# Optimization experiments

Measured on AMD Instinct MI355X. Metric: run time of the kernel, lower is better.

The kernel has to match this reference:

```python
import jax, jax.numpy as jnp
import numpy as np

GN_EPS = 1e-5
LN_EPS = 1e-5
M_HEADS, N_LEVELS, N_POINTS, D_MODEL = 8, 3, 4, 256
HEAD_DIM = D_MODEL // M_HEADS


def conv1x1(x, w, b):
    return jnp.einsum('nchw,oc->nohw', x, w[:, :, 0, 0]) + b[None, :, None, None]


def conv3x3(x, w, b):
    y = jax.lax.conv_general_dilated(x, w, (1, 1), ((1, 1), (1, 1)),
                                     dimension_numbers=('NCHW', 'OIHW', 'NCHW'))
    return y + b[None, :, None, None]


def group_norm(x, w, b, groups=32):
    N, C, H, W = x.shape
    xg = x.reshape(N, groups, C // groups, H, W)
    mu = xg.mean((2, 3, 4), keepdims=True)
    var = xg.var((2, 3, 4), keepdims=True)
    xg = (xg - mu) / jnp.sqrt(var + GN_EPS)
    return xg.reshape(N, C, H, W) * w[None, :, None, None] + b[None, :, None, None]


def layer_norm(x, w, b):
    mu = x.mean(-1, keepdims=True)
    var = x.var(-1, keepdims=True)
    return (x - mu) / jnp.sqrt(var + LN_EPS) * w + b


def prelu(x, a):
    return jnp.where(x >= 0, x, a[0] * x)


def pos_sine(mask):
    # DETR PositionEmbeddingSine, num_pos_feats=128, normalize=True
    nm = (~mask).astype(jnp.float32)
    y_embed = jnp.cumsum(nm, 1)
    x_embed = jnp.cumsum(nm, 2)
    eps, scale = 1e-6, 2.0 * np.pi
    y_embed = y_embed / (y_embed[:, -1:, :] + eps) * scale
    x_embed = x_embed / (x_embed[:, :, -1:] + eps) * scale
    npf = D_MODEL // 2
    dim_t = 10000.0 ** (2.0 * (jnp.arange(npf) // 2).astype(jnp.float32) / npf)
    px = x_embed[..., None] / dim_t
    py = y_embed[..., None] / dim_t

    def il(p):
        return jnp.stack([jnp.sin(p[..., 0::2]), jnp.cos(p[..., 1::2])], -1).reshape(p.shape[0], p.shape[1], p.shape[2], -1)

    return jnp.transpose(jnp.concatenate([il(py), il(px)], -1), (0, 3, 1, 2))


def resize_mask_nearest(mask, h, w):
    H, W = mask.shape[1], mask.shape[2]
    iy = jnp.floor(jnp.arange(h) * (H / h)).astype(jnp.int32)
    ix = jnp.floor(jnp.arange(w) * (W / w)).astype(jnp.int32)
    return mask[:, iy][:, :, ix]


def bilinear_gather(v, x, y):
    # v: (N,M,D,H,W); x,y: (N,Lq,M,P) pixel coords; zero padding, align_corners=False
    N, M, D, H, W = v.shape
    Lq, P = x.shape[1], x.shape[3]
    x0f = jnp.floor(x)
    y0f = jnp.floor(y)
    wx = (x - x0f)[..., None]
    wy = (y - y0f)[..., None]
    x0i = x0f.astype(jnp.int32)
    y0i = y0f.astype(jnp.int32)
    flat = jnp.transpose(v, (0, 1, 3, 4, 2)).reshape(N, M, H * W, D)

    def gather(xi, yi):
        valid = (xi >= 0) & (xi < W) & (yi >= 0) & (yi < H)
        idx = jnp.clip(yi, 0, H - 1) * W + jnp.clip(xi, 0, W - 1)
        idx2 = jnp.transpose(idx, (0, 2, 1, 3)).reshape(N, M, Lq * P)
        g = jnp.take_along_axis(flat, idx2[..., None], axis=2)
        g = jnp.transpose(g.reshape(N, M, Lq, P, D), (0, 2, 1, 3, 4))
        return g * valid[..., None]

    g00 = gather(x0i, y0i)
    g01 = gather(x0i + 1, y0i)
    g10 = gather(x0i, y0i + 1)
    g11 = gather(x0i + 1, y0i + 1)
    return g00 * (1 - wx) * (1 - wy) + g01 * wx * (1 - wy) + g10 * (1 - wx) * wy + g11 * wx * wy


def _forward(x0, x1, x2, p3_w, p3_b, p4_w, p4_b, p5_w, p5_b,
             gn3_w, gn3_b, gn4_w, gn4_b, gn5_w, gn5_b, level_embed,
             so_w, so_b, aw_w, aw_b, vp_w, vp_b, op_w, op_b,
             ln1_w, ln1_b, ffn1_w, ffn1_b, ffn2_w, ffn2_b, ln2_w, ln2_b,
             d3_w, d3_b, d3_a, d4_w, d4_b, d4_a, d5_w, d5_b, d5_a,
             padding_masks):
    N = x0.shape[0]
    shapes = [(x0.shape[2], x0.shape[3]), (x1.shape[2], x1.shape[3]), (x2.shape[2], x2.shape[3])]
    p3 = group_norm(conv1x1(x0, p3_w, p3_b), gn3_w, gn3_b)
    p4 = group_norm(conv1x1(x1, p4_w, p4_b), gn4_w, gn4_b)
    p5 = group_norm(conv1x1(x2, p5_w, p5_b), gn5_w, gn5_b)
    srcs = [p3, p4, p5]
    masks = [resize_mask_nearest(padding_masks, H, W) for (H, W) in shapes]
    src_flat = jnp.concatenate([s.reshape(N, D_MODEL, -1).transpose(0, 2, 1) for s in srcs], 1)
    mask_flat = jnp.concatenate([m.reshape(N, -1) for m in masks], 1)
    pos_flat = jnp.concatenate(
        [pos_sine(m).reshape(N, D_MODEL, -1).transpose(0, 2, 1) + level_embed[l][None, None]
         for l, m in enumerate(masks)], 1)
    # valid ratios (N, 3, 2) as (w, h)
    vrs = []
    for (H, W), m in zip(shapes, masks):
        vh = jnp.sum((~m[:, :, 0]).astype(jnp.float32), 1) / H
        vw = jnp.sum((~m[:, 0, :]).astype(jnp.float32), 1) / W
        vrs.append(jnp.stack([vw, vh], -1))
    vr = jnp.stack(vrs, 1)
    # reference points (N, Lq, 3, 2)
    refs = []
    for lvl, (H, W) in enumerate(shapes):
        ry, rx = jnp.meshgrid(jnp.linspace(0.5, H - 0.5, H), jnp.linspace(0.5, W - 0.5, W), indexing='ij')
        ry = ry.reshape(-1)[None] / (vr[:, None, lvl, 1] * H)
        rx = rx.reshape(-1)[None] / (vr[:, None, lvl, 0] * W)
        refs.append(jnp.stack([rx, ry], -1))
    ref = jnp.concatenate(refs, 1)[:, :, None] * vr[:, None]

    # --- MSDeformAttn ---
    q = src_flat + pos_flat
    Lq = q.shape[1]
    value = src_flat @ vp_w.T + vp_b
    value = jnp.where(mask_flat[..., None], 0.0, value).reshape(N, Lq, M_HEADS, HEAD_DIM)
    off = (q @ so_w.T + so_b).reshape(N, Lq, M_HEADS, N_LEVELS, N_POINTS, 2)
    aw = jax.nn.softmax((q @ aw_w.T + aw_b).reshape(N, Lq, M_HEADS, N_LEVELS * N_POINTS), -1)
    aw = aw.reshape(N, Lq, M_HEADS, N_LEVELS, N_POINTS)
    norm = jnp.array([[W, H] for (H, W) in shapes], jnp.float32)
    loc = ref[:, :, None, :, None, :] + off / norm[None, None, None, :, None, :]
    out = jnp.zeros((N, Lq, M_HEADS, HEAD_DIM), value.dtype)
    start = 0
    for l, (H, W) in enumerate(shapes):
        vl = value[:, start:start + H * W].reshape(N, H, W, M_HEADS, HEAD_DIM)
        vl = jnp.transpose(vl, (0, 3, 4, 1, 2))  # (N, M, D, H, W)
        sx = loc[:, :, :, l, :, 0] * W - 0.5
        sy = loc[:, :, :, l, :, 1] * H - 0.5
        samp = bilinear_gather(vl, sx, sy)  # (N, Lq, M, P, D)
        out = out + jnp.einsum('nqmpd,nqmp->nqmd', samp, aw[:, :, :, l])
        start += H * W
    attn = out.reshape(N, Lq, D_MODEL) @ op_w.T + op_b

    src = layer_norm(src_flat + attn, ln1_w, ln1_b)
    ffn = jax.nn.relu(src @ ffn1_w.T + ffn1_b) @ ffn2_w.T + ffn2_b
    src = layer_norm(src + ffn, ln2_w, ln2_b)

    # take level-2 tokens back to spatial
    H2, W2 = shapes[2]
    start2 = shapes[0][0] * shapes[0][1] + shapes[1][0] * shapes[1][1]
    o = src[:, start2:start2 + H2 * W2].reshape(N, H2, W2, D_MODEL).transpose(0, 3, 1, 2)

    o = jax.image.resize(o, (N, D_MODEL) + shapes[0], 'bilinear', antialias=False) + prelu(conv3x3(x0, d3_w, d3_b), d3_a)
    o = jax.image.resize(o, (N, D_MODEL) + shapes[1], 'bilinear', antialias=False) + prelu(conv3x3(x1, d4_w, d4_b), d4_a)
    o = jax.image.resize(o, (N, D_MODEL) + shapes[2], 'bilinear', antialias=False) + prelu(conv3x3(x2, d5_w, d5_b), d5_a)
    return o


def setup_inputs():
    key = jax.random.key(0)
    ks = jax.random.split(key, 24)
    B, C = 2, 256

    def w(k, shape, sc=0.02):
        return jax.random.normal(k, shape, jnp.float32) * sc

    inp = {}
    inp['x0'] = jax.random.normal(ks[0], (B, 2048, 64, 64), jnp.float32)
    inp['x1'] = jax.random.normal(ks[1], (B, 2048, 32, 32), jnp.float32)
    inp['x2'] = jax.random.normal(ks[2], (B, 2048, 16, 16), jnp.float32)
    inp['padding_masks'] = jnp.zeros((B, 64, 64), bool)
    inp['p3_w'] = w(ks[3], (C, 2048, 1, 1)); inp['p3_b'] = jnp.zeros((C,))
    inp['p4_w'] = w(ks[4], (C, 2048, 1, 1)); inp['p4_b'] = jnp.zeros((C,))
    inp['p5_w'] = w(ks[5], (C, 2048, 1, 1)); inp['p5_b'] = jnp.zeros((C,))
    inp['gn3_w'] = jnp.ones((C,)); inp['gn3_b'] = jnp.zeros((C,))
    inp['gn4_w'] = jnp.ones((C,)); inp['gn4_b'] = jnp.zeros((C,))
    inp['gn5_w'] = jnp.ones((C,)); inp['gn5_b'] = jnp.zeros((C,))
    inp['level_embed'] = w(ks[6], (3, C), 1.0)
    inp['so_w'] = w(ks[7], (192, C)); inp['so_b'] = w(ks[8], (192,), 0.5)
    inp['aw_w'] = w(ks[9], (96, C)); inp['aw_b'] = jnp.zeros((96,))
    inp['vp_w'] = w(ks[10], (C, C)); inp['vp_b'] = jnp.zeros((C,))
    inp['op_w'] = w(ks[11], (C, C)); inp['op_b'] = jnp.zeros((C,))
    inp['ln1_w'] = jnp.ones((C,)); inp['ln1_b'] = jnp.zeros((C,))
    inp['ffn1_w'] = w(ks[12], (1024, C)); inp['ffn1_b'] = jnp.zeros((1024,))
    inp['ffn2_w'] = w(ks[13], (C, 1024)); inp['ffn2_b'] = jnp.zeros((C,))
    inp['ln2_w'] = jnp.ones((C,)); inp['ln2_b'] = jnp.zeros((C,))
    inp['d3_w'] = w(ks[14], (C, 2048, 3, 3)); inp['d3_b'] = jnp.zeros((C,)); inp['d3_a'] = jnp.full((1,), 0.25)
    inp['d4_w'] = w(ks[15], (C, 2048, 3, 3)); inp['d4_b'] = jnp.zeros((C,)); inp['d4_a'] = jnp.full((1,), 0.25)
    inp['d5_w'] = w(ks[16], (C, 2048, 3, 3)); inp['d5_b'] = jnp.zeros((C,)); inp['d5_a'] = jnp.full((1,), 0.25)
    return inp


def reference(x0, x1, x2, padding_masks, p3_w, p3_b, p4_w, p4_b, p5_w, p5_b,
              gn3_w, gn3_b, gn4_w, gn4_b, gn5_w, gn5_b, level_embed,
              so_w, so_b, aw_w, aw_b, vp_w, vp_b, op_w, op_b,
              ln1_w, ln1_b, ffn1_w, ffn1_b, ffn2_w, ffn2_b, ln2_w, ln2_b,
              d3_w, d3_b, d3_a, d4_w, d4_b, d4_a, d5_w, d5_b, d5_a):
    return _forward(x0, x1, x2, p3_w, p3_b, p4_w, p4_b, p5_w, p5_b,
                    gn3_w, gn3_b, gn4_w, gn4_b, gn5_w, gn5_b, level_embed,
                    so_w, so_b, aw_w, aw_b, vp_w, vp_b, op_w, op_b,
                    ln1_w, ln1_b, ffn1_w, ffn1_b, ffn2_w, ffn2_b, ln2_w, ln2_b,
                    d3_w, d3_b, d3_a, d4_w, d4_b, d4_a, d5_w, d5_b, d5_a,
                    padding_masks)
```

## Files before the change

kernel.cpp:

```cpp
#include <hip/hip_runtime.h>
#include <hip/hip_bf16.h>

#define NTOK 5376

typedef short bfrag __attribute__((ext_vector_type(8)));
typedef short bvec4 __attribute__((ext_vector_type(4)));
typedef float facc  __attribute__((ext_vector_type(4)));

__device__ __forceinline__ short f2bf(float f) {
  __hip_bfloat16 h = __float2bfloat16(f);
  return *reinterpret_cast<short*>(&h);
}
__device__ __forceinline__ float bf2f(short s) {
  union { unsigned int u; float f; } cv;
  cv.u = ((unsigned int)(unsigned short)s) << 16;
  return cv.f;
}

#define ASYNC_COPY16(gp, sp) \
  __builtin_amdgcn_global_load_lds((const __attribute__((address_space(1))) unsigned int*)(gp), \
                                   (__attribute__((address_space(3))) unsigned int*)(sp), 16, 0, 0)

__global__ __launch_bounds__(256) void init_all_kernel(
    const float* __restrict__ x0, const float* __restrict__ x1, const float* __restrict__ x2,
    short* __restrict__ xb0, short* __restrict__ xb1, short* __restrict__ xb2,
    const float* __restrict__ p3, const float* __restrict__ p4, const float* __restrict__ p5,
    const float* __restrict__ vp,
    const float* __restrict__ so, const float* __restrict__ aw, const float* __restrict__ op,
    const float* __restrict__ f1, const float* __restrict__ f2,
    const float* __restrict__ d3,
    short* __restrict__ pwb0, short* __restrict__ pwb1, short* __restrict__ pwb2,
    short* __restrict__ vpb,
    short* __restrict__ soT, short* __restrict__ awT, short* __restrict__ opT,
    short* __restrict__ f1T, short* __restrict__ f2T,
    short* __restrict__ w0)
{
  __shared__ __align__(16) float tileF[64 * 68];
  __shared__ float tt[32][33];
  int b = blockIdx.x;
  if (b < 7168) {
    const float* x; short* xb; int H, Wshift;
    if (b < 4096)      { x = x0; xb = xb0; H = 64; Wshift = 6; }
    else if (b < 6144) { x = x1; xb = xb1; H = 32; Wshift = 5; b -= 4096; }
    else               { x = x2; xb = xb2; H = 16; Wshift = 4; b -= 6144; }
    int cin0 = (b & 31) << 6;
    int t1 = b >> 5;
    int y = t1 & (H - 1);
    int n = t1 >> Wshift;
    int W = 1 << Wshift;
    int HW = H * W;
    int Wq = W >> 2;
    const float* xrow = x + ((long)(n * 2048 + cin0) * H + y) * W;
    int units1 = 64 * Wq;
    for (int e = threadIdx.x; e < units1; e += 256) {
      int row = e >> (Wshift - 2);
      int c4 = (e & (Wq - 1)) << 2;
      float4 v = *(const float4*)(xrow + (long)row * HW + c4);
      *(float4*)(&tileF[row * 68 + c4]) = v;
    }
    __syncthreads();
    int Hp = H + 2;
    short* orow = xb + (((long)(n * Hp + y + 1)) * Hp + 1) * 2048 + cin0;
    int units2 = W * 8;
    for (int e = threadIdx.x; e < units2; e += 256) {
      int px = e >> 3, g = e & 7;
      bfrag o;
#pragma unroll
      for (int j = 0; j < 8; ++j) o[j] = f2bf(tileF[(g * 8 + j) * 68 + px]);
      *(bfrag*)(orow + (long)px * 2048 + g * 8) = o;
    }
    return;
  }
  b -= 7168;
  if (b < 6144) {
    const float* src; short* dst;
    if (b < 2048)      { src = p3; dst = pwb0; }
    else if (b < 4096) { src = p4; dst = pwb1; b -= 2048; }
    else               { src = p5; dst = pwb2; b -= 4096; }
    int idx = b * 256 + threadIdx.x;
    dst[idx] = f2bf(src[idx]);
    return;
  }
  b -= 6144;
  if (b < 256) {
    int idx = b * 256 + threadIdx.x;
    vpb[idx] = f2bf(vp[idx]);
    return;
  }
  b -= 256;
  if (b < 648) {
    const float* src; short* dst; int N, K, tb;
    if (b < 48)       { src = so; dst = soT; N = 192;  K = 256;  tb = b; }
    else if (b < 72)  { src = aw; dst = awT; N = 96;   K = 256;  tb = b - 48; }
    else if (b < 136) { src = op; dst = opT; N = 256;  K = 256;  tb = b - 72; }
    else if (b < 392) { src = f1; dst = f1T; N = 1024; K = 256;  tb = b - 136; }
    else              { src = f2; dst = f2T; N = 256;  K = 1024; tb = b - 392; }
    int ktiles = K >> 5;
    int tn = tb / ktiles, tk = tb % ktiles;
#pragma unroll
    for (int s = 0; s < 4; ++s) {
      int i = s * 256 + threadIdx.x;
      int r = i >> 5, c = i & 31;
      tt[r][c] = src[(long)(tn * 32 + r) * K + tk * 32 + c];
    }
    __syncthreads();
#pragma unroll
    for (int s = 0; s < 4; ++s) {
      int i = s * 256 + threadIdx.x;
      int r = i >> 5, c = i & 31;
      dst[(long)(tk * 32 + r) * N + tn * 32 + c] = f2bf(tt[c][r]);
    }
    return;
  }
  b -= 648;
  if (b < 2048) {
    int p = b * 256 + threadIdx.x;
    int oc = p >> 11, cin = p & 2047;
    float v[9];
#pragma unroll
    for (int t = 0; t < 9; ++t) v[t] = d3[(long)p * 9 + t];
#pragma unroll
    for (int ky = 0; ky < 3; ++ky)
#pragma unroll
      for (int kx = 0; kx < 3; ++kx)
        w0[((long)(ky * 256 + oc)) * 6144 + kx * 2048 + cin] = f2bf(v[ky * 3 + kx]);
    return;
  }
  b -= 2048;
  {
    int zb = b;
    short* xb; int Hp, cnt2;
    if (zb < 33)      { xb = xb0; Hp = 66; cnt2 = 260; }
    else if (zb < 50) { xb = xb1; Hp = 34; cnt2 = 132; zb -= 33; }
    else              { xb = xb2; Hp = 18; cnt2 = 68;  zb -= 50; }
    bfrag z = (bfrag)(short)0;
    int total = 2 * cnt2;
    for (int k = 0; k < 16; ++k) {
      int fi = zb * 16 + k;
      if (fi >= total) break;
      int n = fi / cnt2;
      int f = fi - n * cnt2;
      int yy, xx;
      if (f < Hp)          { yy = 0;      xx = f; }
      else if (f < 2 * Hp) { yy = Hp - 1; xx = f - Hp; }
      else { int r = f - 2 * Hp; yy = 1 + (r >> 1); xx = (r & 1) ? (Hp - 1) : 0; }
      *(bfrag*)(xb + (((long)(n * Hp + yy)) * Hp + xx) * 2048 + threadIdx.x * 8) = z;
    }
  }
}

__global__ __launch_bounds__(256) void convert_w12_kernel(
    const float* __restrict__ d4, const float* __restrict__ d5,
    short* __restrict__ w1, short* __restrict__ w2) {
  int b = blockIdx.x;
  const float* src; short* dst;
  if (b < 2048) { src = d4; dst = w1; } else { src = d5; dst = w2; b -= 2048; }
  int p = b * 256 + threadIdx.x;
  int oc = p >> 11, cin = p & 2047;
  float v[9];
#pragma unroll
  for (int t = 0; t < 9; ++t) v[t] = src[(long)p * 9 + t];
#pragma unroll
  for (int ky = 0; ky < 3; ++ky)
#pragma unroll
    for (int kx = 0; kx < 3; ++kx)
      dst[((long)(ky * 256 + oc)) * 6144 + kx * 2048 + cin] = f2bf(v[ky * 3 + kx]);
}

#define BUF3 24576

__device__ __forceinline__ void conv3x3_pipe3(short* lds,
    const short* __restrict__ xb, const short* __restrict__ wb,
    short* __restrict__ part, int Wshift, int HW2, int mt, int kb, int T)
{
  int tid = threadIdx.x;
  int lane = tid & 63;
  int wid = tid >> 6;
  int wm = wid >> 2;
  int wn = wid & 3;
  int W = 1 << Wshift;
  int HW = 1 << (2 * Wshift);
  int px0 = mt * 128;
  int n = px0 >> (2 * Wshift);
  int rem = px0 & (HW - 1);
  int Hp = W + 2;
  long rowstride = (long)Hp * 2048;

  const short* ag[2];
#pragma unroll
  for (int r = 0; r < 2; ++r) {
    int c = r * 512 + tid;
    int pl = c >> 3;
    int kc = (c & 7) ^ (pl & 7);
    int p = rem + pl;
    int yy = p >> Wshift, xx = p & (W - 1);
    ag[r] = xb + (((long)(n * Hp + yy)) * Hp + xx) * 2048 + kc * 8;
  }
  const short* bg[4];
#pragma unroll
  for (int r = 0; r < 4; ++r) {
    int c = r * 512 + tid;
    int pl = c >> 3;
    int kc = (c & 7) ^ (pl & 7);
    bg[r] = wb + (long)pl * 6144 + kc * 8;
  }
  int ldst = (tid & 448) * 8;

  int arow[4], brow[4];
#pragma unroll
  for (int i = 0; i < 4; ++i) {
    arow[i] = (wm * 64 + i * 16 + (lane & 15)) * 64;
    brow[i] = 8192 + (i * 64 + wn * 16 + (lane & 15)) * 64;
  }
  int kcs[2];
#pragma unroll
  for (int k0 = 0; k0 < 2; ++k0)
    kcs[k0] = ((((k0 << 2) + (lane >> 4)) ^ (lane & 7)) << 3);

  facc acc[4][4];
#pragma unroll
  for (int mi = 0; mi < 4; ++mi)
#pragma unroll
    for (int ni = 0; ni < 4; ++ni) acc[mi][ni] = (facc)(0.f);

  auto KYOFF = [&](int it, long& ao, long& bo) {
    int ky = (it >= 192) ? 2 : ((it >= 96) ? 1 : 0);
    int kc96 = it - ky * 96;
    ao = (long)ky * rowstride + (long)kc96 * 64;
    bo = (long)ky * 1572864 + (long)kc96 * 64;
  };
  auto ISSUE_A = [&](int it, int bufi) {
    long ao, bo; KYOFF(it, ao, bo); (void)bo;
    short* db = lds + bufi * BUF3;
    ASYNC_COPY16(ag[0] + ao, db + ldst);
    ASYNC_COPY16(ag[1] + ao, db + 4096 + ldst);
  };
  auto ISSUE_B0 = [&](int it, int bufi) {
    long ao, bo; KYOFF(it, ao, bo); (void)ao;
    short* db = lds + bufi * BUF3;
    ASYNC_COPY16(bg[0] + bo, db + 8192 + ldst);
    ASYNC_COPY16(bg[1] + bo, db + 12288 + ldst);
  };
  auto ISSUE_B1 = [&](int it, int bufi) {
    long ao, bo; KYOFF(it, ao, bo); (void)ao;
    short* db = lds + bufi * BUF3;
    ASYNC_COPY16(bg[2] + bo, db + 16384 + ldst);
    ASYNC_COPY16(bg[3] + bo, db + 20480 + ldst);
  };

  auto RD_A = [&](int bufi, int k0, bfrag* af) {
    const short* buf = lds + bufi * BUF3;
#pragma unroll
    for (int mi = 0; mi < 4; ++mi) af[mi] = *(const bfrag*)(buf + arow[mi] + kcs[k0]);
  };
  auto RD_B = [&](int bufi, int k0, int nh, bfrag* bf) {
    const short* buf = lds + bufi * BUF3;
#pragma unroll
    for (int j = 0; j < 2; ++j) bf[j] = *(const bfrag*)(buf + brow[2 * nh + j] + kcs[k0]);
  };
  auto MM = [&](bfrag* af, bfrag* bf, int nh) {
    __builtin_amdgcn_s_setprio(1);
#pragma unroll
    for (int mi = 0; mi < 4; ++mi)
#pragma unroll
      for (int j = 0; j < 2; ++j)
        acc[mi][2 * nh + j] = __builtin_amdgcn_mfma_f32_16x16x32_bf16(af[mi], bf[j], acc[mi][2 * nh + j], 0, 0, 0);
    __builtin_amdgcn_s_setprio(0);
  };

  int it0 = kb * T;
  bfrag a0[4], a1[4], b0[2], b1[2];

  ISSUE_A(it0 + 0, 0); ISSUE_B0(it0 + 0, 0); ISSUE_B1(it0 + 0, 0);
  ISSUE_A(it0 + 1, 1); ISSUE_B0(it0 + 1, 1); ISSUE_B1(it0 + 1, 1);
  asm volatile("s_waitcnt vmcnt(8)" ::: "memory");
  __builtin_amdgcn_s_barrier();

  int cur = 0;
  for (int t = 0; t < T - 2; ++t) {
    int nxt = cur + 2; if (nxt >= 3) nxt -= 3;
    int itn = it0 + t + 2;
    RD_A(cur, 0, a0); RD_B(cur, 0, 0, b0);
    ISSUE_A(itn, nxt);
    MM(a0, b0, 0);
    RD_A(cur, 1, a1); RD_B(cur, 1, 0, b1);
    ISSUE_B0(itn, nxt);
    MM(a1, b1, 0);
    asm volatile("s_waitcnt vmcnt(10)" ::: "memory");
    __builtin_amdgcn_s_barrier();
    RD_B(cur, 0, 1, b0);
    ISSUE_B1(itn, nxt);
    MM(a0, b0, 1);
    RD_B(cur, 1, 1, b1);
    MM(a1, b1, 1);
    asm volatile("s_waitcnt vmcnt(8)" ::: "memory");
    __builtin_amdgcn_s_barrier();
    if (++cur == 3) cur = 0;
  }
  {
    RD_A(cur, 0, a0); RD_B(cur, 0, 0, b0); MM(a0, b0, 0);
    RD_A(cur, 1, a1); RD_B(cur, 1, 0, b1); MM(a1, b1, 0);
    asm volatile("s_waitcnt vmcnt(6)" ::: "memory");
    __builtin_amdgcn_s_barrier();
    RD_B(cur, 0, 1, b0); MM(a0, b0, 1);
    RD_B(cur, 1, 1, b1); MM(a1, b1, 1);
    asm volatile("s_waitcnt vmcnt(2)" ::: "memory");
    __builtin_amdgcn_s_barrier();
    if (++cur == 3) cur = 0;
  }
  {
    RD_A(cur, 0, a0); RD_B(cur, 0, 0, b0); MM(a0, b0, 0);
    RD_A(cur, 1, a1); RD_B(cur, 1, 0, b1); MM(a1, b1, 0);
    asm volatile("s_waitcnt vmcnt(0)" ::: "memory");
    __builtin_amdgcn_s_barrier();
    RD_B(cur, 0, 1, b0); MM(a0, b0, 1);
    RD_B(cur, 1, 1, b1); MM(a1, b1, 1);
  }

  short* pp = part + ((long)kb * HW2 + px0) * 256;
#pragma unroll
  for (int mi = 0; mi < 4; ++mi) {
    int pl = wm * 64 + mi * 16 + ((lane >> 4) << 2);
#pragma unroll
    for (int nj = 0; nj < 4; ++nj) {
      int ol = nj * 64 + wn * 16 + (lane & 15);
#pragma unroll
      for (int r = 0; r < 4; ++r)
        pp[(long)(pl + r) * 256 + ol] = f2bf(acc[mi][nj][r]);
    }
  }
}

__global__ __launch_bounds__(512, 2) void conv0_kernel(
    const short* __restrict__ xb, const short* __restrict__ wb, short* __restrict__ part) {
  __shared__ __align__(16) short lds[3 * BUF3];
  int b = blockIdx.x;
  conv3x3_pipe3(lds, xb, wb, part, 6, 8192, b >> 2, b & 3, 72);
}

__device__ __forceinline__ void reduce_tile32(int bb, const short* __restrict__ part,
    const float* __restrict__ bias, const float* __restrict__ alpha_p,
    short* __restrict__ out, int HW2, int hwshift, int KB) {
  int px0 = bb * 32;
  int n = px0 >> hwshift;
  int sp0 = px0 & ((1 << hwshift) - 1);
  int oc0 = (threadIdx.x & 31) * 8;
  int pr  = threadIdx.x >> 5;
  long step = (long)HW2 * 256;
  float acc[4][8];
#pragma unroll
  for (int ii = 0; ii < 4; ++ii)
#pragma unroll
    for (int c = 0; c < 8; ++c) acc[ii][c] = 0.f;
  for (int kb = 0; kb < KB; ++kb) {
#pragma unroll
    for (int ii = 0; ii < 4; ++ii) {
      int px = px0 + pr * 4 + ii;
      bfrag v = *(const bfrag*)(part + kb * step + (long)px * 256 + oc0);
#pragma unroll
      for (int c = 0; c < 8; ++c) acc[ii][c] += bf2f(v[c]);
    }
  }
  float alpha = alpha_p[0];
#pragma unroll
  for (int c = 0; c < 8; ++c) {
    float bs = bias[oc0 + c];
    bvec4 o;
#pragma unroll
    for (int ii = 0; ii < 4; ++ii) {
      float v = acc[ii][c] + bs;
      v = (v >= 0.f) ? v : alpha * v;
      o[ii] = f2bf(v);
    }
    *(bvec4*)(out + (((long)(n * 256 + oc0 + c)) << hwshift) + sp0 + pr * 4) = o;
  }
}

__device__ __forceinline__ void reduce_tile64(int bb, const short* __restrict__ part,
    const float* __restrict__ bias, const float* __restrict__ alpha_p,
    short* __restrict__ out, int HW2, int hwshift, int KB) {
  int px0 = bb * 64;
  int n = px0 >> hwshift;
  int sp0 = px0 & ((1 << hwshift) - 1);
  int oc0 = (threadIdx.x & 31) * 8;
  int pr  = threadIdx.x >> 5;
  long step = (long)HW2 * 256;
  float acc[4][8];
#pragma unroll
  for (int ii = 0; ii < 4; ++ii)
#pragma unroll
    for (int c = 0; c < 8; ++c) acc[ii][c] = 0.f;
  for (int kb = 0; kb < KB; ++kb) {
#pragma unroll
    for (int ii = 0; ii < 4; ++ii) {
      int px = px0 + pr * 4 + ii;
      bfrag v = *(const bfrag*)(part + kb * step + (long)px * 256 + oc0);
#pragma unroll
      for (int c = 0; c < 8; ++c) acc[ii][c] += bf2f(v[c]);
    }
  }
  float alpha = alpha_p[0];
#pragma unroll
  for (int c = 0; c < 8; ++c) {
    float bs = bias[oc0 + c];
    bvec4 o;
#pragma unroll
    for (int ii = 0; ii < 4; ++ii) {
      float v = acc[ii][c] + bs;
      v = (v >= 0.f) ? v : alpha * v;
      o[ii] = f2bf(v);
    }
    *(bvec4*)(out + (((long)(n * 256 + oc0 + c)) << hwshift) + sp0 + pr * 4) = o;
  }
}

__global__ __launch_bounds__(512, 2) void conv12_fused_kernel(
    const short* __restrict__ xb1, const short* __restrict__ w1, short* __restrict__ part1,
    const short* __restrict__ xb2, const short* __restrict__ w2, short* __restrict__ part2,
    const short* __restrict__ part0, const float* __restrict__ d3_b,
    const float* __restrict__ d3_a, short* __restrict__ c0b,
    const short* __restrict__ srcb, float* __restrict__ stats) {
  __shared__ __align__(16) short lds[3 * BUF3];
  int b = blockIdx.x;
  if (b < 128) { conv3x3_pipe3(lds, xb1, w1, part1, 5, 2048, b >> 3, b & 7, 36); return; }
  if (b < 160) { b -= 128; conv3x3_pipe3(lds, xb2, w2, part2, 4, 512, b >> 3, b & 7, 36); return; }
  if (b < 288) { reduce_tile64(b - 160, part0, d3_b, d3_a, c0b, 8192, 12, 4); return; }
  int sb = b - 288;
  int n = sb / 96, r = sb % 96, l = r / 32, g = r % 32;
  int H, base;
  if (l == 0)      { H = 64; base = 0; }
  else if (l == 1) { H = 32; base = 4096; }
  else             { H = 16; base = 5120; }
  int HW = H * H;
  const short* p = srcb + ((long)n * NTOK + base) * 256 + g * 8;
  int tid = threadIdx.x;
  float s = 0.f, s2 = 0.f;
  if (tid < 256) {
    for (int idx = tid; idx < HW * 8; idx += 256) {
      int hw = idx >> 3, c = idx & 7;
      float v = bf2f(p[(long)hw * 256 + c]);
      s += v; s2 += v * v;
    }
  }
#pragma unroll
  for (int o = 32; o > 0; o >>= 1) {
    s  += __shfl_down(s, o, 64);
    s2 += __shfl_down(s2, o, 64);
  }
  float* r1 = (float*)lds;
  float* r2 = r1 + 8;
  int wid = tid >> 6, lane = tid & 63;
  if (lane == 0 && wid < 4) { r1[wid] = s; r2[wid] = s2; }
  __syncthreads();
  if (tid == 0) {
    float ss  = r1[0] + r1[1] + r1[2] + r1[3];
    float ss2 = r2[0] + r2[1] + r2[2] + r2[3];
    float cnt = (float)(HW * 8);
    float mu = ss / cnt;
    float var = ss2 / cnt - mu * mu;
    stats[sb * 2]     = mu;
    stats[sb * 2 + 1] = rsqrtf(var + 1e-5f);
  }
}

__global__ __launch_bounds__(256) void gn_apply_kernel(short* __restrict__ srcb,
    const float* __restrict__ stats,
    const float* __restrict__ gw0, const float* __restrict__ gb0,
    const float* __restrict__ gw1, const float* __restrict__ gb1,
    const float* __restrict__ gw2, const float* __restrict__ gb2) {
  long i8 = ((long)blockIdx.x * 256 + threadIdx.x) * 8;
  int row = (int)(i8 >> 8), c0 = (int)(i8 & 255);
  int n = row / NTOK, t = row % NTOK;
  int l; const float *gw, *gb;
  if (t < 4096)      { l = 0; gw = gw0; gb = gb0; }
  else if (t < 5120) { l = 1; gw = gw1; gb = gb1; }
  else               { l = 2; gw = gw2; gb = gb2; }
  int si = (n * 96 + l * 32 + (c0 >> 3)) * 2;
  float mu = stats[si], rstd = stats[si + 1];
  bfrag v = *(bfrag*)(srcb + i8);
  bfrag o;
#pragma unroll
  for (int j = 0; j < 8; ++j)
    o[j] = f2bf((bf2f(v[j]) - mu) * rstd * gw[c0 + j] + gb[c0 + j]);
  *(bfrag*)(srcb + i8) = o;
}

__device__ __forceinline__ void block_reduce2(float& s, float& s2) {
#pragma unroll
  for (int o = 32; o > 0; o >>= 1) {
    s  += __shfl_down(s, o, 64);
    s2 += __shfl_down(s2, o, 64);
  }
  __shared__ float r1[4], r2[4];
  int wid = threadIdx.x >> 6;
  int lane = threadIdx.x & 63;
  if (lane == 0) { r1[wid] = s; r2[wid] = s2; }
  __syncthreads();
  s  = r1[0] + r1[1] + r1[2] + r1[3];
  s2 = r2[0] + r2[1] + r2[2] + r2[3];
  __syncthreads();
}

#define BUFC 20480

__global__ __launch_bounds__(512, 2) void conv1x1_all_kernel(
    const short* __restrict__ xb0, const short* __restrict__ xb1, const short* __restrict__ xb2,
    const short* __restrict__ pwb0, const short* __restrict__ pwb1, const short* __restrict__ pwb2,
    const float* __restrict__ p3_b, const float* __restrict__ p4_b, const float* __restrict__ p5_b,
    short* __restrict__ srcb)
{
  __shared__ __align__(16) short lds[3 * BUFC];
  int b = blockIdx.x;
  const short* A; const short* Bw; const float* bias;
  int Wshift, Hp, shift2, tokbase, py;
  if (b < 128)      { A = xb0; Bw = pwb0; bias = p3_b; Wshift = 6; Hp = 66; shift2 = 12; tokbase = 0;    py = b; }
  else if (b < 160) { A = xb1; Bw = pwb1; bias = p4_b; Wshift = 5; Hp = 34; shift2 = 10; tokbase = 4096; py = b - 128; }
  else              { A = xb2; Bw = pwb2; bias = p5_b; Wshift = 4; Hp = 18; shift2 = 8;  tokbase = 5120; py = b - 160; }

  int tid = threadIdx.x;
  int lane = tid & 63;
  int wid = tid >> 6;
  int wm = wid >> 2, wn = wid & 3;
  int px0 = py * 64;
  int W = 1 << Wshift;

  const short* ag;
  {
    int pl = tid >> 3;
    int kc = (tid & 7) ^ (pl & 7);
    int p = px0 + pl;
    int n = p >> shift2;
    int remp = p & ((1 << shift2) - 1);
    int yy = remp >> Wshift, xx = remp & (W - 1);
    ag = A + (((long)(n * Hp + yy + 1)) * Hp + (xx + 1)) * 2048 + kc * 8;
  }
  const short* bg[4];
#pragma unroll
  for (int r = 0; r < 4; ++r) {
    int c = r * 512 + tid;
    int pl = c >> 3;
    int kc = (c & 7) ^ (pl & 7);
    bg[r] = Bw + (long)pl * 2048 + kc * 8;
  }
  int ldst = (tid & 448) * 8;

  int arow[2], brow[4];
#pragma unroll
  for (int i = 0; i < 2; ++i) arow[i] = (wm * 32 + i * 16 + (lane & 15)) * 64;
#pragma unroll
  for (int i = 0; i < 4; ++i) brow[i] = 4096 + (i * 64 + wn * 16 + (lane & 15)) * 64;
  int kcs[2];
#pragma unroll
  for (int k0 = 0; k0 < 2; ++k0)
    kcs[k0] = ((((k0 << 2) + (lane >> 4)) ^ (lane & 7)) << 3);

  facc acc[2][4];
#pragma unroll
  for (int mi = 0; mi < 2; ++mi)
#pragma unroll
    for (int ni = 0; ni < 4; ++ni) acc[mi][ni] = (facc)(0.f);

  auto ISSUE_A = [&](int it, int bufi) {
    short* db = lds + bufi * BUFC;
    ASYNC_COPY16(ag + (long)it * 64, db + ldst);
  };
  auto ISSUE_B0 = [&](int it, int bufi) {
    short* db = lds + bufi * BUFC;
    ASYNC_COPY16(bg[0] + (long)it * 64, db + 4096 + ldst);
    ASYNC_COPY16(bg[1] + (long)it * 64, db + 8192 + ldst);
  };
  auto ISSUE_B1 = [&](int it, int bufi) {
    short* db = lds + bufi * BUFC;
    ASYNC_COPY16(bg[2] + (long)it * 64, db + 12288 + ldst);
    ASYNC_COPY16(bg[3] + (long)it * 64, db + 16384 + ldst);
  };
  auto RD_A = [&](int bufi, int k0, bfrag* af) {
    const short* buf = lds + bufi * BUFC;
#pragma unroll
    for (int mi = 0; mi < 2; ++mi) af[mi] = *(const bfrag*)(buf + arow[mi] + kcs[k0]);
  };
  auto RD_B = [&](int bufi, int k0, int nh, bfrag* bf) {
    const short* buf = lds + bufi * BUFC;
#pragma unroll
    for (int j = 0; j < 2; ++j) bf[j] = *(const bfrag*)(buf + brow[2 * nh + j] + kcs[k0]);
  };
  auto MM = [&](bfrag* af, bfrag* bf, int nh) {
    __builtin_amdgcn_s_setprio(1);
#pragma unroll
    for (int mi = 0; mi < 2; ++mi)
#pragma unroll
      for (int j = 0; j < 2; ++j)
        acc[mi][2 * nh + j] = __builtin_amdgcn_mfma_f32_16x16x32_bf16(af[mi], bf[j], acc[mi][2 * nh + j], 0, 0, 0);
    __builtin_amdgcn_s_setprio(0);
  };

  bfrag a0[2], a1[2], b0[2], b1[2];

  ISSUE_A(0, 0); ISSUE_B0(0, 0); ISSUE_B1(0, 0);
  ISSUE_A(1, 1); ISSUE_B0(1, 1); ISSUE_B1(1, 1);
  asm volatile("s_waitcnt vmcnt(7)" ::: "memory");
  __builtin_amdgcn_s_barrier();

  int cur = 0;
  for (int t = 0; t < 30; ++t) {
    int nxt = cur + 2; if (nxt >= 3) nxt -= 3;
    int itn = t + 2;
    RD_A(cur, 0, a0); RD_B(cur, 0, 0, b0);
    ISSUE_A(itn, nxt);
    MM(a0, b0, 0);
    RD_A(cur, 1, a1); RD_B(cur, 1, 0, b1);
    ISSUE_B0(itn, nxt);
    MM(a1, b1, 0);
    asm volatile("s_waitcnt vmcnt(8)" ::: "memory");
    __builtin_amdgcn_s_barrier();
    RD_B(cur, 0, 1, b0);
    ISSUE_B1(itn, nxt);
    MM(a0, b0, 1);
    RD_B(cur, 1, 1, b1);
    MM(a1, b1, 1);
    asm volatile("s_waitcnt vmcnt(7)" ::: "memory");
    __builtin_amdgcn_s_barrier();
    if (++cur == 3) cur = 0;
  }
  {
    RD_A(cur, 0, a0); RD_B(cur, 0, 0, b0); MM(a0, b0, 0);
    RD_A(cur, 1, a1); RD_B(cur, 1, 0, b1); MM(a1, b1, 0);
    asm volatile("s_waitcnt vmcnt(5)" ::: "memory");
    __builtin_amdgcn_s_barrier();
    RD_B(cur, 0, 1, b0); MM(a0, b0, 1);
    RD_B(cur, 1, 1, b1); MM(a1, b1, 1);
    asm volatile("s_waitcnt vmcnt(2)" ::: "memory");
    __builtin_amdgcn_s_barrier();
    if (++cur == 3) cur = 0;
  }
  {
    RD_A(cur, 0, a0); RD_B(cur, 0, 0, b0); MM(a0, b0, 0);
    RD_A(cur, 1, a1); RD_B(cur, 1, 0, b1); MM(a1, b1, 0);
    asm volatile("s_waitcnt vmcnt(0)" ::: "memory");
    __builtin_amdgcn_s_barrier();
    RD_B(cur, 0, 1, b0); MM(a0, b0, 1);
    RD_B(cur, 1, 1, b1); MM(a1, b1, 1);
  }

#pragma unroll
  for (int mi = 0; mi < 2; ++mi) {
    int plb = wm * 32 + mi * 16 + ((lane >> 4) << 2);
#pragma unroll
    for (int r = 0; r < 4; ++r) {
      int row = px0 + plb + r;
      int n = row >> shift2;
      int tl = row & ((1 << shift2) - 1);
      long rowoff = ((long)(n * NTOK + tokbase + tl)) * 256;
#pragma unroll
      for (int nj = 0; nj < 4; ++nj) {
        int col = nj * 64 + wn * 16 + (lane & 15);
        srcb[rowoff + col] = f2bf(acc[mi][nj][r] + bias[col]);
      }
    }
  }
}

__global__ __launch_bounds__(256) void valproj_kernel(
    const short* __restrict__ A, const short* __restrict__ Bw,
    const float* __restrict__ bias, float* __restrict__ Cf) {
  __shared__ __align__(16) short As[128 * 64];
  __shared__ __align__(16) short Bs[128 * 64];
  int tid = threadIdx.x;
  int lane = tid & 63;
  int wid = tid >> 6;
  int wm = wid >> 1, wn = wid & 1;
  int px0 = blockIdx.y * 128;
  int ocb = blockIdx.x;

  const short* ag0[4];
  const short* bg0[4];
#pragma unroll
  for (int j = 0; j < 4; ++j) {
    int c = j * 256 + tid;
    int pl = c >> 3;
    int kc = (c & 7) ^ (pl & 7);
    ag0[j] = A + (long)(px0 + pl) * 256 + kc * 8;
    bg0[j] = Bw + (long)(ocb * 128 + pl) * 256 + kc * 8;
  }

  facc acc[4][4];
#pragma unroll
  for (int mi = 0; mi < 4; ++mi)
#pragma unroll
    for (int ni = 0; ni < 4; ++ni) acc[mi][ni] = (facc)(0.f);

  for (int it = 0; it < 4; ++it) {
    long off = (long)it * 64;
#pragma unroll
    for (int j = 0; j < 4; ++j) {
      ASYNC_COPY16(ag0[j] + off, As + (j * 256 + (tid & 192)) * 8);
      ASYNC_COPY16(bg0[j] + off, Bs + (j * 256 + (tid & 192)) * 8);
    }
    __syncthreads();
#pragma unroll
    for (int k0 = 0; k0 < 2; ++k0) {
      bfrag af[4], bf[4];
      int kc = ((k0 << 2) + (lane >> 4)) ^ (lane & 7);
#pragma unroll
      for (int mi = 0; mi < 4; ++mi) {
        int ml = wm * 64 + mi * 16 + (lane & 15);
        af[mi] = *(const bfrag*)(As + ml * 64 + kc * 8);
      }
#pragma unroll
      for (int ni = 0; ni < 4; ++ni) {
        int nl = wn * 64 + ni * 16 + (lane & 15);
        bf[ni] = *(const bfrag*)(Bs + nl * 64 + kc * 8);
      }
#pragma unroll
      for (int mi = 0; mi < 4; ++mi)
#pragma unroll
        for (int ni = 0; ni < 4; ++ni)
          acc[mi][ni] = __builtin_amdgcn_mfma_f32_16x16x32_bf16(af[mi], bf[ni], acc[mi][ni], 0, 0, 0);
    }
    __syncthreads();
  }

#pragma unroll
  for (int mi = 0; mi < 4; ++mi) {
    int plb = wm * 64 + mi * 16 + ((lane >> 4) << 2);
#pragma unroll
    for (int r = 0; r < 4; ++r) {
      long rowoff = (long)(px0 + plb + r) * 256;
#pragma unroll
// ... 308 lines not shown
```

Before: 492.1 us.

## Load conv A operand directly to registers and swizzle init transpose tile

The 3x3 conv GEMM no longer stages the activation (A) tile through LDS. Each lane loads its A fragments straight from global memory into registers, double-buffered across even and odd iterations, while only the weight (B) tile goes through the 3-stage async LDS ring. This shrinks the LDS footprint and cuts LDS traffic and barrier phases, at the cost of more registers and uncoalesced direct global loads for A. Separately, the fp32 transpose tile in the init kernel gets an XOR swizzle to reduce bank conflicts.

```diff
diff --git a/kernel.cpp b/kernel.cpp
--- a/kernel.cpp
+++ b/kernel.cpp
@@ -20,6 +20,8 @@
 #define ASYNC_COPY16(gp, sp) \
   __builtin_amdgcn_global_load_lds((const __attribute__((address_space(1))) unsigned int*)(gp), \
                                    (__attribute__((address_space(3))) unsigned int*)(sp), 16, 0, 0)
+
+#define TIX(r, c) ((r) * 68 + ((c) ^ ((((r) >> 3) & 7) << 2)))
 
 __global__ __launch_bounds__(256) void init_all_kernel(
     const float* __restrict__ x0, const float* __restrict__ x1, const float* __restrict__ x2,
@@ -56,7 +58,7 @@
       int row = e >> (Wshift - 2);
       int c4 = (e & (Wq - 1)) << 2;
       float4 v = *(const float4*)(xrow + (long)row * HW + c4);
-      *(float4*)(&tileF[row * 68 + c4]) = v;
+      *(float4*)(&tileF[TIX(row, c4)]) = v;
     }
     __syncthreads();
     int Hp = H + 2;
@@ -66,7 +68,7 @@
       int px = e >> 3, g = e & 7;
       bfrag o;
 #pragma unroll
-      for (int j = 0; j < 8; ++j) o[j] = f2bf(tileF[(g * 8 + j) * 68 + px]);
+      for (int j = 0; j < 8; ++j) o[j] = f2bf(tileF[TIX(g * 8 + j, px)]);
       *(bfrag*)(orow + (long)px * 2048 + g * 8) = o;
     }
     return;
@@ -167,9 +169,9 @@
       dst[((long)(ky * 256 + oc)) * 6144 + kx * 2048 + cin] = f2bf(v[ky * 3 + kx]);
 }
 
-#define BUF3 24576
-
-__device__ __forceinline__ void conv3x3_pipe3(short* lds,
+#define BUFB 16384
+
+__device__ __forceinline__ void conv3x3_pipe4(short* lds,
     const short* __restrict__ xb, const short* __restrict__ wb,
     short* __restrict__ part, int Wshift, int HW2, int mt, int kb, int T)
 {
@@ -186,16 +188,6 @@
   int Hp = W + 2;
   long rowstride = (long)Hp * 2048;
 
-  const short* ag[2];
-#pragma unroll
-  for (int r = 0; r < 2; ++r) {
-    int c = r * 512 + tid;
-    int pl = c >> 3;
-    int kc = (c & 7) ^ (pl & 7);
-    int p = rem + pl;
-    int yy = p >> Wshift, xx = p & (W - 1);
-    ag[r] = xb + (((long)(n * Hp + yy)) * Hp + xx) * 2048 + kc * 8;
-  }
   const short* bg[4];
 #pragma unroll
   for (int r = 0; r < 4; ++r) {
@@ -206,12 +198,18 @@
   }
   int ldst = (tid & 448) * 8;
 
-  int arow[4], brow[4];
-#pragma unroll
-  for (int i = 0; i < 4; ++i) {
-    arow[i] = (wm * 64 + i * 16 + (lane & 15)) * 64;
-    brow[i] = 8192 + (i * 64 + wn * 16 + (lane & 15)) * 64;
-  }
+  const short* aR[4];
+#pragma unroll
+  for (int mi = 0; mi < 4; ++mi) {
+    int p = rem + wm * 64 + mi * 16 + (lane & 15);
+    int yy = p >> Wshift, xx = p & (W - 1);
+    aR[mi] = xb + (((long)(n * Hp + yy)) * Hp + xx) * 2048 + (lane >> 4) * 8;
+  }
+
+  int brow[4];
+#pragma unroll
+  for (int i = 0; i < 4; ++i)
+    brow[i] = (i * 64 + wn * 16 + (lane & 15)) * 64;
   int kcs[2];
 #pragma unroll
   for (int k0 = 0; k0 < 2; ++k0)
@@ -229,93 +227,76 @@
     ao = (long)ky * rowstride + (long)kc96 * 64;
     bo = (long)ky * 1572864 + (long)kc96 * 64;
   };
-  auto ISSUE_A = [&](int it, int bufi) {
+  auto ISSUE_B = [&](int it, int bufi) {
+    long ao, bo; KYOFF(it, ao, bo); (void)ao;
+    short* db = lds + bufi * BUFB;
+    ASYNC_COPY16(bg[0] + bo, db + ldst);
+    ASYNC_COPY16(bg[1] + bo, db + 4096 + ldst);
+    ASYNC_COPY16(bg[2] + bo, db + 8192 + ldst);
+    ASYNC_COPY16(bg[3] + bo, db + 12288 + ldst);
+  };
+  auto LOAD_A = [&](int it, bfrag* af) {
     long ao, bo; KYOFF(it, ao, bo); (void)bo;
-    short* db = lds + bufi * BUF3;
-    ASYNC_COPY16(ag[0] + ao, db + ldst);
-    ASYNC_COPY16(ag[1] + ao, db + 4096 + ldst);
+#pragma unroll
+    for (int k0 = 0; k0 < 2; ++k0)
+#pragma unroll
+      for (int mi = 0; mi < 4; ++mi)
+        af[k0 * 4 + mi] = *(const bfrag*)(aR[mi] + ao + k0 * 32);
   };
-  auto ISSUE_B0 = [&](int it, int bufi) {
-    long ao, bo; KYOFF(it, ao, bo); (void)ao;
-    short* db = lds + bufi * BUF3;
-    ASYNC_COPY16(bg[0] + bo, db + 8192 + ldst);
-    ASYNC_COPY16(bg[1] + bo, db + 12288 + ldst);
+  auto COMPUTE = [&](int bufi, bfrag* af) {
+    const short* buf = lds + bufi * BUFB;
+#pragma unroll
+    for (int nh = 0; nh < 2; ++nh) {
+#pragma unroll
+      for (int k0 = 0; k0 < 2; ++k0) {
+        bfrag bf[2];
+#pragma unroll
+        for (int j = 0; j < 2; ++j)
+          bf[j] = *(const bfrag*)(buf + brow[2 * nh + j] + kcs[k0]);
+        __builtin_amdgcn_s_setprio(1);
+#pragma unroll
+        for (int mi = 0; mi < 4; ++mi)
+#pragma unroll
+          for (int j = 0; j < 2; ++j)
+            acc[mi][2 * nh + j] = __builtin_amdgcn_mfma_f32_16x16x32_bf16(
+                af[k0 * 4 + mi], bf[j], acc[mi][2 * nh + j], 0, 0, 0);
+        __builtin_amdgcn_s_setprio(0);
+      }
+    }
   };
-  auto ISSUE_B1 = [&](int it, int bufi) {
-    long ao, bo; KYOFF(it, ao, bo); (void)ao;
-    short* db = lds + bufi * BUF3;
-    ASYNC_COPY16(bg[2] + bo, db + 16384 + ldst);
-    ASYNC_COPY16(bg[3] + bo, db + 20480 + ldst);
-  };
-
-  auto RD_A = [&](int bufi, int k0, bfrag* af) {
-    const short* buf = lds + bufi * BUF3;
-#pragma unroll
-    for (int mi = 0; mi < 4; ++mi) af[mi] = *(const bfrag*)(buf + arow[mi] + kcs[k0]);
-  };
-  auto RD_B = [&](int bufi, int k0, int nh, bfrag* bf) {
-    const short* buf = lds + bufi * BUF3;
-#pragma unroll
-    for (int j = 0; j < 2; ++j) bf[j] = *(const bfrag*)(buf + brow[2 * nh + j] + kcs[k0]);
-  };
-  auto MM = [&](bfrag* af, bfrag* bf, int nh) {
-    __builtin_amdgcn_s_setprio(1);
-#pragma unroll
-    for (int mi = 0; mi < 4; ++mi)
-#pragma unroll
-      for (int j = 0; j < 2; ++j)
-        acc[mi][2 * nh + j] = __builtin_amdgcn_mfma_f32_16x16x32_bf16(af[mi], bf[j], acc[mi][2 * nh + j], 0, 0, 0);
-    __builtin_amdgcn_s_setprio(0);
-  };
 
   int it0 = kb * T;
-  bfrag a0[4], a1[4], b0[2], b1[2];
-
-  ISSUE_A(it0 + 0, 0); ISSUE_B0(it0 + 0, 0); ISSUE_B1(it0 + 0, 0);
-  ISSUE_A(it0 + 1, 1); ISSUE_B0(it0 + 1, 1); ISSUE_B1(it0 + 1, 1);
+  bfrag afE[8], afO[8];
+
+  ISSUE_B(it0 + 0, 0);
+  ISSUE_B(it0 + 1, 1);
+  LOAD_A(it0 + 0, afE);
+  asm volatile("s_waitcnt vmcnt(12)" ::: "memory");
+  __builtin_amdgcn_s_barrier();
+
+  int cur = 0;
+  for (int t = 0; t + 3 < T; t += 2) {
+    int nb = cur + 2; if (nb >= 3) nb -= 3;
+    ISSUE_B(it0 + t + 2, nb);
+    LOAD_A(it0 + t + 1, afO);
+    COMPUTE(cur, afE);
+    asm volatile("s_waitcnt vmcnt(12)" ::: "memory");
+    __builtin_amdgcn_s_barrier();
+    if (++cur == 3) cur = 0;
+    nb = cur + 2; if (nb >= 3) nb -= 3;
+    ISSUE_B(it0 + t + 3, nb);
+    LOAD_A(it0 + t + 2, afE);
+    COMPUTE(cur, afO);
+    asm volatile("s_waitcnt vmcnt(12)" ::: "memory");
+    __builtin_amdgcn_s_barrier();
+    if (++cur == 3) cur = 0;
+  }
+  LOAD_A(it0 + T - 1, afO);
+  COMPUTE(cur, afE);
   asm volatile("s_waitcnt vmcnt(8)" ::: "memory");
   __builtin_amdgcn_s_barrier();
-
-  int cur = 0;
-  for (int t = 0; t < T - 2; ++t) {
-    int nxt = cur + 2; if (nxt >= 3) nxt -= 3;
-    int itn = it0 + t + 2;
-    RD_A(cur, 0, a0); RD_B(cur, 0, 0, b0);
-    ISSUE_A(itn, nxt);
-    MM(a0, b0, 0);
-    RD_A(cur, 1, a1); RD_B(cur, 1, 0, b1);
-    ISSUE_B0(itn, nxt);
-    MM(a1, b1, 0);
-    asm volatile("s_waitcnt vmcnt(10)" ::: "memory");
-    __builtin_amdgcn_s_barrier();
-    RD_B(cur, 0, 1, b0);
-    ISSUE_B1(itn, nxt);
-    MM(a0, b0, 1);
-    RD_B(cur, 1, 1, b1);
-    MM(a1, b1, 1);
-    asm volatile("s_waitcnt vmcnt(8)" ::: "memory");
-    __builtin_amdgcn_s_barrier();
-    if (++cur == 3) cur = 0;
-  }
-  {
-    RD_A(cur, 0, a0); RD_B(cur, 0, 0, b0); MM(a0, b0, 0);
-    RD_A(cur, 1, a1); RD_B(cur, 1, 0, b1); MM(a1, b1, 0);
-    asm volatile("s_waitcnt vmcnt(6)" ::: "memory");
-    __builtin_amdgcn_s_barrier();
-    RD_B(cur, 0, 1, b0); MM(a0, b0, 1);
-    RD_B(cur, 1, 1, b1); MM(a1, b1, 1);
-    asm volatile("s_waitcnt vmcnt(2)" ::: "memory");
-    __builtin_amdgcn_s_barrier();
-    if (++cur == 3) cur = 0;
-  }
-  {
-    RD_A(cur, 0, a0); RD_B(cur, 0, 0, b0); MM(a0, b0, 0);
-    RD_A(cur, 1, a1); RD_B(cur, 1, 0, b1); MM(a1, b1, 0);
-    asm volatile("s_waitcnt vmcnt(0)" ::: "memory");
-    __builtin_amdgcn_s_barrier();
-    RD_B(cur, 0, 1, b0); MM(a0, b0, 1);
-    RD_B(cur, 1, 1, b1); MM(a1, b1, 1);
-  }
+  if (++cur == 3) cur = 0;
+  COMPUTE(cur, afO);
 
   short* pp = part + ((long)kb * HW2 + px0) * 256;
 #pragma unroll
@@ -333,9 +314,9 @@
 
 __global__ __launch_bounds__(512, 2) void conv0_kernel(
     const short* __restrict__ xb, const short* __restrict__ wb, short* __restrict__ part) {
-  __shared__ __align__(16) short lds[3 * BUF3];
+  __shared__ __align__(16) short lds[3 * BUFB];
   int b = blockIdx.x;
-  conv3x3_pipe3(lds, xb, wb, part, 6, 8192, b >> 2, b & 3, 72);
+  conv3x3_pipe4(lds, xb, wb, part, 6, 8192, b >> 2, b & 3, 72);
 }
 
 __device__ __forceinline__ void reduce_tile32(int bb, const short* __restrict__ part,
@@ -420,10 +401,10 @@
     const short* __restrict__ part0, const float* __restrict__ d3_b,
     const float* __restrict__ d3_a, short* __restrict__ c0b,
     const short* __restrict__ srcb, float* __restrict__ stats) {
-  __shared__ __align__(16) short lds[3 * BUF3];
+  __shared__ __align__(16) short lds[3 * BUFB];
   int b = blockIdx.x;
-  if (b < 128) { conv3x3_pipe3(lds, xb1, w1, part1, 5, 2048, b >> 3, b & 7, 36); return; }
-  if (b < 160) { b -= 128; conv3x3_pipe3(lds, xb2, w2, part2, 4, 512, b >> 3, b & 7, 36); return; }
+  if (b < 128) { conv3x3_pipe4(lds, xb1, w1, part1, 5, 2048, b >> 3, b & 7, 36); return; }
+  if (b < 160) { b -= 128; conv3x3_pipe4(lds, xb2, w2, part2, 4, 512, b >> 3, b & 7, 36); return; }
   if (b < 288) { reduce_tile64(b - 160, part0, d3_b, d3_a, c0b, 8192, 12, 4); return; }
   int sb = b - 288;
   int n = sb / 96, r = sb % 96, l = r / 32, g = r % 32;
```

Result: slower. 626.0 us (+27.2%).
